# Kernel tuning notes

Hardware: AMD Instinct MI355X
Metric: run time of the kernel (lower is better)

## Reference

```python
import jax, jax.numpy as jnp
import numpy as np

N = 20000        # number of protein atoms
C_IN = 32        # input atom features
C = 128          # hidden_channels
E_BOND = 80000   # directed bond edges (~2 bonds/atom, both directions)
R = 4.0          # radius_graph radius (Angstrom)
BOX = 55.0       # box side -> ~32 neighbors within r=4


def _radius_graph_np(pos, r):
    # symmetric radius graph, no self loops (PyG radius_graph, neighbor cap omitted)
    r2 = r * r
    rows, cols = [], []
    for i0 in range(0, pos.shape[0], 500):
        chunk = pos[i0:i0 + 500]
        d2 = ((chunk[:, None, :] - pos[None, :, :]) ** 2).sum(-1)
        m = d2 < r2
        m[np.arange(chunk.shape[0]), i0 + np.arange(chunk.shape[0])] = False
        ii, jj = np.nonzero(m)
        rows.append(jj)            # source j
        cols.append(ii + i0)       # target i
    return np.stack([np.concatenate(rows), np.concatenate(cols)]).astype(np.int32)


def setup_inputs() -> dict:
    key = jax.random.key(0)
    ks = jax.random.split(key, 12)
    rng = np.random.default_rng(0)

    pos = rng.uniform(0.0, BOX, (N, 3)).astype(np.float32)
    r_edge_index = jnp.asarray(_radius_graph_np(pos, R))

    half = E_BOND // 2
    s = rng.integers(0, N, half); d = rng.integers(0, N, half)
    edge_index = jnp.asarray(np.stack([np.concatenate([s, d]), np.concatenate([d, s])]).astype(np.int32))

    def lin(k, fin, fout):
        lim = 1.0 / np.sqrt(fin)
        kw, kb = jax.random.split(k)
        W = jax.random.uniform(kw, (fin, fout), jnp.float32, -lim, lim)
        b = jax.random.uniform(kb, (fout,), jnp.float32, -lim, lim)
        return W, b

    We1, be1 = lin(ks[0], C_IN, C)
    We2, be2 = lin(ks[1], C, C)
    Wf1, bf1 = lin(ks[2], 2 * C, C); Ws1, bs1 = lin(ks[3], 2 * C, C)
    Wf2, bf2 = lin(ks[4], 2 * C, C); Ws2, bs2 = lin(ks[5], 2 * C, C)
    Wf3, bf3 = lin(ks[6], 2 * C, C); Ws3, bs3 = lin(ks[7], 2 * C, C)
    Wf4, bf4 = lin(ks[8], 2 * C, C); Ws4, bs4 = lin(ks[9], 2 * C, C)

    x_prot = jax.random.normal(ks[10], (N, C_IN), jnp.float32)
    v_prot = jnp.asarray(pos)

    return dict(x_prot=x_prot, v_prot=v_prot, edge_index=edge_index, r_edge_index=r_edge_index,
                We1=We1, be1=be1, We2=We2, be2=be2,
                Wf1=Wf1, bf1=bf1, Ws1=Ws1, bs1=bs1,
                Wf2=Wf2, bf2=bf2, Ws2=Ws2, bs2=bs2,
                Wf3=Wf3, bf3=bf3, Ws3=Ws3, bs3=bs3,
                Wf4=Wf4, bf4=bf4, Ws4=Ws4, bs4=bs4)


def _cgconv(x, ei, Wf, bf, Ws, bs):
    # PyG CGConv: z = [x_i, x_j]; out = x + mean_j sigmoid(lin_f(z)) * softplus(lin_s(z))
    src, dst = ei[0], ei[1]              # source j -> target i
    z = jnp.concatenate([x[dst], x[src]], axis=1)          # [E, 2C]
    msg = jax.nn.sigmoid(z @ Wf + bf) * jax.nn.softplus(z @ Ws + bs)  # [E, C]
    agg = jax.ops.segment_sum(msg, dst, num_segments=x.shape[0])
    cnt = jax.ops.segment_sum(jnp.ones((ei.shape[1],), x.dtype), dst, num_segments=x.shape[0])
    return x + agg / jnp.maximum(cnt, 1.0)[:, None]


def reference(x_prot, v_prot, edge_index, r_edge_index,
              We1, be1, We2, be2,
              Wf1, bf1, Ws1, bs1, Wf2, bf2, Ws2, bs2,
              Wf3, bf3, Ws3, bs3, Wf4, bf4, Ws4, bs4):
    # embed MLP (PyG MLP with batch-norm at init == identity): Linear->ReLU->Linear
    x = jax.nn.relu(x_prot @ We1 + be1) @ We2 + be2
    # bond convs
    x = jax.nn.relu(_cgconv(x, edge_index, Wf1, bf1, Ws1, bs1))
    x = jax.nn.relu(_cgconv(x, edge_index, Wf2, bf2, Ws2, bs2))
    # radius convs (r_edge_index = radius_graph(v_prot, r=4), precomputed in setup)
    x = jax.nn.relu(_cgconv(x, r_edge_index, Wf3, bf3, Ws3, bs3))
    x = jax.nn.relu(_cgconv(x, r_edge_index, Wf4, bf4, Ws4, bs4))
    return jax.nn.relu(x)  # final self.act (idempotent on ReLU output)
```

## Files before the change

kernel.cpp:

```cpp
#include <hip/hip_runtime.h>
#include <hip/hip_bf16.h>

#define NN 20000
#define CC 128

typedef __attribute__((ext_vector_type(8))) _Float16 half8;
typedef __attribute__((ext_vector_type(2))) _Float16 half2v;
typedef __attribute__((ext_vector_type(4))) float f32x4;

typedef const __attribute__((address_space(1))) void gv_t;
typedef __attribute__((address_space(3))) void sv_t;

__global__ __launch_bounds__(256) void conv_all_kernel(
    const float* __restrict__ Wf0, const float* __restrict__ Ws0,
    const float* __restrict__ Wf1, const float* __restrict__ Ws1,
    const float* __restrict__ Wf2, const float* __restrict__ Ws2,
    const float* __restrict__ Wf3, const float* __restrict__ Ws3,
    const float* __restrict__ We2, const float* __restrict__ We1,
    const float* __restrict__ xprot,
    _Float16* __restrict__ WctAll, _Float16* __restrict__ Wcte,
    _Float16* __restrict__ Wt1, _Float16* __restrict__ xp16) {
    int id = blockIdx.x * 256 + threadIdx.x;
    if (id < 262144) {
        int Lw = id >> 16;
        int i = id & 65535;
        int c = i & 511;
        int k = i >> 9;
        const float* Wfp = (Lw == 0) ? Wf0 : (Lw == 1) ? Wf1 : (Lw == 2) ? Wf2 : Wf3;
        const float* Wsp = (Lw == 0) ? Ws0 : (Lw == 1) ? Ws1 : (Lw == 2) ? Ws2 : Ws3;
        float v;
        if (c < 128) v = Wfp[k * 128 + c];
        else if (c < 256) v = Wfp[(128 + k) * 128 + (c - 128)];
        else if (c < 384) v = Wsp[k * 128 + (c - 256)];
        else v = Wsp[(128 + k) * 128 + (c - 384)];
        WctAll[Lw * 65536 + c * 128 + k] = (_Float16)v;
    } else if (id < 278528) {
        int i = id - 262144;
        int c = i & 127;
        int k = i >> 7;
        Wcte[c * 128 + k] = (_Float16)We2[k * 128 + c];
    } else if (id < 282624) {
        int i = id - 278528;
        int c = i & 127;
        int k = i >> 7;
        Wt1[c * 32 + k] = (_Float16)We1[k * 128 + c];
    } else {
        int i = id - 282624;
        xp16[i] = (_Float16)xprot[i];
    }
}

__global__ __launch_bounds__(256) void enc1_mfma_kernel(
    const _Float16* __restrict__ A, const _Float16* __restrict__ Wt1,
    const float* __restrict__ b, _Float16* __restrict__ Y) {
    int t = threadIdx.x;
    int wid = t >> 6, l = t & 63;
    int lr = l & 15, hi = l >> 4;
    int m0 = blockIdx.x * 128 + wid * 32;
    half8 af[2];
#pragma unroll
    for (int m = 0; m < 2; ++m) {
        int row = m0 + m * 16 + lr;
        half8 v = {0, 0, 0, 0, 0, 0, 0, 0};
        if (row < NN) v = *(const half8*)(A + (long)row * 32 + hi * 8);
        af[m] = v;
    }
    f32x4 acc[2][8] = {};
#pragma unroll
    for (int n = 0; n < 8; ++n) {
        int col = n * 16 + lr;
        half8 bg = *(const half8*)(Wt1 + (long)col * 32 + hi * 8);
#pragma unroll
        for (int m = 0; m < 2; ++m)
            acc[m][n] = __builtin_amdgcn_mfma_f32_16x16x32_f16(af[m], bg, acc[m][n], 0, 0, 0);
    }
#pragma unroll
    for (int n = 0; n < 8; ++n) {
        int col = n * 16 + lr;
        float bb = b[col];
#pragma unroll
        for (int m = 0; m < 2; ++m) {
#pragma unroll
            for (int q = 0; q < 4; ++q) {
                int row = m0 + m * 16 + hi * 4 + q;
                if (row < NN)
                    Y[(long)row * 128 + col] = (_Float16)fmaxf(acc[m][n][q] + bb, 0.0f);
            }
        }
    }
}

__global__ __launch_bounds__(256) void gemm_mfma_kernel(
    const _Float16* __restrict__ A, const _Float16* __restrict__ Wt,
    const float* __restrict__ bias0, const float* __restrict__ bias1,
    _Float16* __restrict__ outH, float* __restrict__ outF,
    _Float16* __restrict__ outF16, int M, int mode) {
    __shared__ _Float16 lds[32768];
    int t = threadIdx.x;
    int w = t >> 6, l = t & 63;
    int m0 = blockIdx.x * 128;
    int n0 = blockIdx.y * 128;
    {
        int rin = l >> 4;
        int cs = l & 15;
#pragma unroll
        for (int j = 0; j < 8; ++j) {
            int r = w * 32 + j * 4 + rin;
            int g = cs ^ (r & 7);
            int grow = m0 + r;
            if (grow > M - 1) grow = M - 1;
            const _Float16* srcA = A + (long)grow * 128 + g * 8;
            __builtin_amdgcn_global_load_lds((gv_t*)srcA,
                (sv_t*)&lds[(w * 32 + j * 4) * 128], 16, 0, 0);
            const _Float16* srcB = Wt + (long)(n0 + r) * 128 + g * 8;
            __builtin_amdgcn_global_load_lds((gv_t*)srcB,
                (sv_t*)&lds[16384 + (w * 32 + j * 4) * 128], 16, 0, 0);
        }
    }
    __syncthreads();
    int wm = w >> 1, wn = w & 1;
    int lr = l & 15, hi = l >> 4;
    f32x4 acc[4][4] = {};
#pragma unroll
    for (int ks = 0; ks < 4; ++ks) {
        int cidx = 4 * ks + hi;
        half8 af[4], bg[4];
#pragma unroll
        for (int m = 0; m < 4; ++m) {
            int row = wm * 64 + m * 16 + lr;
            af[m] = *(const half8*)(&lds[row * 128 + (cidx ^ (row & 7)) * 8]);
        }
#pragma unroll
        for (int n = 0; n < 4; ++n) {
            int row = wn * 64 + n * 16 + lr;
            bg[n] = *(const half8*)(&lds[16384 + row * 128 + (cidx ^ (row & 7)) * 8]);
        }
#pragma unroll
        for (int m = 0; m < 4; ++m)
#pragma unroll
            for (int n = 0; n < 4; ++n)
                acc[m][n] = __builtin_amdgcn_mfma_f32_16x16x32_f16(
                    af[m], bg[n], acc[m][n], 0, 0, 0);
    }
    if (mode == 0) {
        __syncthreads();
        const float S = 1.44269504f;
#pragma unroll
        for (int n = 0; n < 4; ++n) {
            int cl = wn * 64 + n * 16 + lr;
            int gcol = n0 + cl;
            float badd = (gcol < 128) ? bias0[gcol]
                       : ((gcol >= 256 && gcol < 384) ? bias1[gcol - 256] : 0.0f);
#pragma unroll
            for (int m = 0; m < 4; ++m)
#pragma unroll
                for (int q = 0; q < 4; ++q) {
                    int rl = wm * 64 + m * 16 + hi * 4 + q;
                    lds[rl * 144 + cl] = (_Float16)((acc[m][n][q] + badd) * S);
                }
        }
        __syncthreads();
#pragma unroll
        for (int i = 0; i < 8; ++i) {
            int id = t + 256 * i;
            int row = id >> 4, ch = id & 15;
            int grow = m0 + row;
            if (grow < M) {
                half8 v = *(const half8*)(&lds[row * 144 + ch * 8]);
                *(half8*)(&outH[(long)grow * 512 + n0 + ch * 8]) = v;
            }
        }
    } else {
#pragma unroll
        for (int n = 0; n < 4; ++n) {
            int gcol = n0 + wn * 64 + n * 16 + lr;
            float badd = bias0[gcol];
#pragma unroll
            for (int m = 0; m < 4; ++m)
#pragma unroll
                for (int q = 0; q < 4; ++q) {
                    int grow = m0 + wm * 64 + m * 16 + hi * 4 + q;
                    if (grow < M) {
                        float v = acc[m][n][q] + badd;
                        outF[(long)grow * 128 + gcol] = v;
                        outF16[(long)grow * 128 + gcol] = (_Float16)v;
                    }
                }
        }
    }
}

__global__ __launch_bounds__(256) void count_int_kernel(
    const int* __restrict__ dst, int E, int* __restrict__ cnt) {
    int e = blockIdx.x * 256 + threadIdx.x;
    if (e < E) atomicAdd(&cnt[dst[e]], 1);
}

__global__ __launch_bounds__(1024) void scan_kernel(
    const int* __restrict__ cnt, int* __restrict__ off) {
    __shared__ int part[1024];
    int t = threadIdx.x;
    int base = t * 20;
    int loc[20];
    int s = 0;
#pragma unroll
    for (int i = 0; i < 20; ++i) {
        int idx = base + i;
        int v = (idx < NN) ? cnt[idx] : 0;
        loc[i] = s;
        s += v;
    }
    part[t] = s;
    __syncthreads();
    for (int d = 1; d < 1024; d <<= 1) {
        int v = (t >= d) ? part[t - d] : 0;
        __syncthreads();
        part[t] += v;
        __syncthreads();
    }
    int pre = (t > 0) ? part[t - 1] : 0;
#pragma unroll
    for (int i = 0; i < 20; ++i) {
        int idx = base + i;
        if (idx < NN) off[idx] = pre + loc[i];
    }
    if (t == 1023) off[NN] = part[1023];
}

__global__ __launch_bounds__(256) void scatter_kernel(
    const int* __restrict__ src, const int* __restrict__ dst, int E,
    const int* __restrict__ off, int* __restrict__ cur, int* __restrict__ eid) {
    int e = blockIdx.x * 256 + threadIdx.x;
    if (e < E) {
        int d = dst[e];
        int p = off[d] + atomicAdd(&cur[d], 1);
        eid[p] = src[e];
    }
}

__global__ __launch_bounds__(256) void csr_off_kernel(
    const int* __restrict__ dst, int E, int N1, int* __restrict__ off) {
    int n = blockIdx.x * 256 + threadIdx.x;
    if (n >= N1) return;
    int lo = 0, hi = E;
    while (lo < hi) {
        int mid = (lo + hi) >> 1;
        if (dst[mid] < n) lo = mid + 1;
        else hi = mid;
    }
    off[n] = lo;
}

__global__ __launch_bounds__(256) void node_agg_kernel(
    const _Float16* __restrict__ H, const int* __restrict__ srcArr,
    const int* __restrict__ off, const float* __restrict__ xin,
    float* __restrict__ xout, _Float16* __restrict__ xh, int write_h) {
    int n = blockIdx.x * 4 + (threadIdx.x >> 6);
    int nu = __builtin_amdgcn_readfirstlane(n);
    int l = threadIdx.x & 63;
    const half2v* H2 = (const half2v*)H;
    const half2v* hrow = H2 + (long)nu * 256;
    half2v fdh = hrow[l];
    half2v sdh = hrow[128 + l];
    int e0 = __builtin_amdgcn_readfirstlane(off[nu]);
    int e1 = __builtin_amdgcn_readfirstlane(off[nu + 1]);
    float ax = 0.0f, ay = 0.0f;
#define EDGEC(fv, sv)                                                         \
    {                                                                         \
        half2v fsum = fdh + (fv);                                             \
        half2v ssum = sdh + (sv);                                             \
        float fx = (float)fsum.x, fy = (float)fsum.y;                         \
        float sx = (float)ssum.x, sy = (float)ssum.y;                         \
        float rx = __builtin_amdgcn_rcpf(1.0f + __builtin_amdgcn_exp2f(-fx)); \
        float ry = __builtin_amdgcn_rcpf(1.0f + __builtin_amdgcn_exp2f(-fy)); \
        float spx = __builtin_amdgcn_logf(1.0f + __builtin_amdgcn_exp2f(sx)); \
        float spy = __builtin_amdgcn_logf(1.0f + __builtin_amdgcn_exp2f(sy)); \
        ax += rx * spx;                                                       \
        ay += ry * spy;                                                       \
    }
    int e = e0;
    for (; e + 7 < e1; e += 8) {
        half2v f[8], g[8];
#pragma unroll
        for (int j = 0; j < 8; ++j) {
            int s = srcArr[e + j];
            const half2v* h = H2 + (long)s * 256;
            f[j] = h[64 + l];
            g[j] = h[192 + l];
        }
#pragma unroll
        for (int j = 0; j < 8; ++j) EDGEC(f[j], g[j])
    }
    for (; e + 1 < e1; e += 2) {
        int s0 = srcArr[e], s1 = srcArr[e + 1];
        const half2v* h0 = H2 + (long)s0 * 256;
        const half2v* h1 = H2 + (long)s1 * 256;
        half2v f0 = h0[64 + l], g0 = h0[192 + l];
        half2v f1 = h1[64 + l], g1 = h1[192 + l];
        EDGEC(f0, g0) EDGEC(f1, g1)
    }
    if (e < e1) {
        int s0 = srcArr[e];
        const half2v* h0 = H2 + (long)s0 * 256;
        half2v f0 = h0[64 + l], g0 = h0[192 + l];
        EDGEC(f0, g0)
    }
#undef EDGEC
    float inv = 0.6931471805599453f *
                __builtin_amdgcn_rcpf(fmaxf((float)(e1 - e0), 1.0f));
    float2 xv = ((const float2*)xin)[(long)nu * 64 + l];
    float ox = fmaxf(xv.x + ax * inv, 0.0f);
    float oy = fmaxf(xv.y + ay * inv, 0.0f);
    ((float2*)xout)[(long)nu * 64 + l] = make_float2(ox, oy);
    if (write_h) {
        half2v oh;
        oh.x = (_Float16)ox;
        oh.y = (_Float16)oy;
        ((half2v*)xh)[(long)nu * 64 + l] = oh;
    }
}

extern "C" void kernel_launch(void* const* d_in, const int* in_sizes, int n_in,
                              void* d_out, int out_size, void* d_ws, size_t ws_size,
                              hipStream_t stream) {
    const float* x_prot = (const float*)d_in[0];
    const int* eb = (const int*)d_in[2];
    const int* er = (const int*)d_in[3];
    int Eb = in_sizes[2] / 2;
    int Er = in_sizes[3] / 2;
    const float* We1 = (const float*)d_in[4];
    const float* be1 = (const float*)d_in[5];
    const float* We2 = (const float*)d_in[6];
    const float* be2 = (const float*)d_in[7];
    const float* Wf[4]  = {(const float*)d_in[8],  (const float*)d_in[12],
                           (const float*)d_in[16], (const float*)d_in[20]};
    const float* bf[4]  = {(const float*)d_in[9],  (const float*)d_in[13],
                           (const float*)d_in[17], (const float*)d_in[21]};
    const float* Wsp[4] = {(const float*)d_in[10], (const float*)d_in[14],
                           (const float*)d_in[18], (const float*)d_in[22]};
    const float* bsp[4] = {(const float*)d_in[11], (const float*)d_in[15],
                           (const float*)d_in[19], (const float*)d_in[23]};

    char* ws = (char*)d_ws;
    float*     xbuf  = (float*)ws;
    _Float16*  xhf   = (_Float16*)(ws + 10240000);
    _Float16*  H     = (_Float16*)(ws + 15360000);
    _Float16*  xp16  = (_Float16*)(ws + 35840000);
    int*       cntI  = (int*)(ws + 37120000);
    int*       curB  = (int*)(ws + 37200000);
    int*       offB  = (int*)(ws + 37280000);
    int*       offR  = (int*)(ws + 37360016);
    int*       eidB  = (int*)(ws + 37440032);
    _Float16*  WctAll= (_Float16*)(ws + 37760032);
    _Float16*  Wcte  = (_Float16*)(ws + 38284320);
    _Float16*  Wt1   = (_Float16*)(ws + 38317088);

    const int* srcB = eb;
    const int* dstB = eb + Eb;
    const int* srcR = er;

    conv_all_kernel<<<3604, 256, 0, stream>>>(
        Wf[0], Wsp[0], Wf[1], Wsp[1], Wf[2], Wsp[2], Wf[3], Wsp[3],
        We2, We1, x_prot, WctAll, Wcte, Wt1, xp16);

    hipMemsetAsync(cntI, 0, 160000, stream);
    count_int_kernel<<<(Eb + 255) / 256, 256, 0, stream>>>(dstB, Eb, cntI);
    scan_kernel<<<1, 1024, 0, stream>>>(cntI, offB);
    scatter_kernel<<<(Eb + 255) / 256, 256, 0, stream>>>(srcB, dstB, Eb, offB, curB, eidB);
    csr_off_kernel<<<(NN + 256) / 256, 256, 0, stream>>>(er + Er, Er, NN + 1, offR);

    enc1_mfma_kernel<<<157, 256, 0, stream>>>(xp16, Wt1, be1, H);
    {
        dim3 g(157, 1);
        gemm_mfma_kernel<<<g, 256, 0, stream>>>(H, Wcte, be2, be2, nullptr,
                                                xbuf, xhf, NN, 1);
    }

    for (int L = 0; L < 4; ++L) {
        dim3 g(157, 4);
        gemm_mfma_kernel<<<g, 256, 0, stream>>>(xhf, WctAll + L * 65536, bf[L],
                                                bsp[L], H, nullptr, nullptr, NN, 0);
        const int* sArr = (L < 2) ? eidB : srcR;
        const int* oArr = (L < 2) ? offB : offR;
        float* xout = (L == 3) ? (float*)d_out : xbuf;
        node_agg_kernel<<<NN / 4, 256, 0, stream>>>(H, sArr, oArr, xbuf, xout,
                                                    xhf, (L == 3) ? 0 : 1);
    }
    (void)n_in; (void)out_size; (void)ws_size;
}
```

Measured before the change: 224.2 us.

## Precompute per-source exp factors in bf16 and factor gate math per edge

The GEMM epilogue now writes the source-side halves of the gate and filter pre-activations as exp2 values rounded to bf16, in a reordered 1024-byte row layout. The node aggregation then computes sigmoid and softplus as rcp(1+ed*es) and log(1+ud*us), with the destination exp computed once per node. This removes two exp2 calls per edge element and reads the B operand directly from global memory into registers with prefetch instead of staging it in LDS, which shrinks the LDS allocation. The risks are bf16 precision on the source factors and possible overflow of the exp values for large pre-activations.

Result: slower. 255.3 us (+13.9%).

```diff
diff --git a/kernel.cpp b/kernel.cpp
--- a/kernel.cpp
+++ b/kernel.cpp
@@ -93,13 +93,22 @@
 __global__ __launch_bounds__(256) void gemm_mfma_kernel(
     const _Float16* __restrict__ A, const _Float16* __restrict__ Wt,
     const float* __restrict__ bias0, const float* __restrict__ bias1,
-    _Float16* __restrict__ outH, float* __restrict__ outF,
+    char* __restrict__ outH, float* __restrict__ outF,
     _Float16* __restrict__ outF16, int M, int mode) {
-    __shared__ _Float16 lds[32768];
+    __shared__ _Float16 lds[18432];
     int t = threadIdx.x;
     int w = t >> 6, l = t & 63;
     int m0 = blockIdx.x * 128;
     int n0 = blockIdx.y * 128;
+    int wm = w >> 1, wn = w & 1;
+    int lr = l & 15, hi = l >> 4;
+    const _Float16* Br[4];
+#pragma unroll
+    for (int n = 0; n < 4; ++n)
+        Br[n] = Wt + (long)(n0 + wn * 64 + n * 16 + lr) * 128 + hi * 8;
+    half8 bcur[4];
+#pragma unroll
+    for (int n = 0; n < 4; ++n) bcur[n] = *(const half8*)(Br[n]);
     {
         int rin = l >> 4;
         int cs = l & 15;
@@ -109,42 +118,43 @@
             int g = cs ^ (r & 7);
             int grow = m0 + r;
             if (grow > M - 1) grow = M - 1;
-            const _Float16* srcA = A + (long)grow * 128 + g * 8;
-            __builtin_amdgcn_global_load_lds((gv_t*)srcA,
+            __builtin_amdgcn_global_load_lds((gv_t*)(A + (long)grow * 128 + g * 8),
                 (sv_t*)&lds[(w * 32 + j * 4) * 128], 16, 0, 0);
-            const _Float16* srcB = Wt + (long)(n0 + r) * 128 + g * 8;
-            __builtin_amdgcn_global_load_lds((gv_t*)srcB,
-                (sv_t*)&lds[16384 + (w * 32 + j * 4) * 128], 16, 0, 0);
         }
     }
     __syncthreads();
-    int wm = w >> 1, wn = w & 1;
-    int lr = l & 15, hi = l >> 4;
     f32x4 acc[4][4] = {};
 #pragma unroll
     for (int ks = 0; ks < 4; ++ks) {
+        half8 bnxt[4];
+        if (ks < 3) {
+#pragma unroll
+            for (int n = 0; n < 4; ++n)
+                bnxt[n] = *(const half8*)(Br[n] + (ks + 1) * 32);
+        }
         int cidx = 4 * ks + hi;
-        half8 af[4], bg[4];
+        half8 af[4];
 #pragma unroll
         for (int m = 0; m < 4; ++m) {
             int row = wm * 64 + m * 16 + lr;
             af[m] = *(const half8*)(&lds[row * 128 + (cidx ^ (row & 7)) * 8]);
         }
 #pragma unroll
-        for (int n = 0; n < 4; ++n) {
-            int row = wn * 64 + n * 16 + lr;
-            bg[n] = *(const half8*)(&lds[16384 + row * 128 + (cidx ^ (row & 7)) * 8]);
-        }
-#pragma unroll
         for (int m = 0; m < 4; ++m)
 #pragma unroll
             for (int n = 0; n < 4; ++n)
                 acc[m][n] = __builtin_amdgcn_mfma_f32_16x16x32_f16(
-                    af[m], bg[n], acc[m][n], 0, 0, 0);
+                    af[m], bcur[n], acc[m][n], 0, 0, 0);
+        if (ks < 3) {
+#pragma unroll
+            for (int n = 0; n < 4; ++n) bcur[n] = bnxt[n];
+        }
     }
     if (mode == 0) {
         __syncthreads();
         const float S = 1.44269504f;
+        bool isSrc = (n0 == 128) || (n0 == 384);
+        float sgn = (n0 == 128) ? -S : S;
 #pragma unroll
         for (int n = 0; n < 4; ++n) {
             int cl = wn * 64 + n * 16 + lr;
@@ -156,10 +166,19 @@
 #pragma unroll
                 for (int q = 0; q < 4; ++q) {
                     int rl = wm * 64 + m * 16 + hi * 4 + q;
-                    lds[rl * 144 + cl] = (_Float16)((acc[m][n][q] + badd) * S);
+                    float v = acc[m][n][q] + badd;
+                    if (!isSrc) {
+                        lds[rl * 144 + cl] = (_Float16)(v * S);
+                    } else {
+                        float p = __builtin_amdgcn_exp2f(v * sgn);
+                        uint b = __float_as_uint(p);
+                        b = (b + 0x7FFFu + ((b >> 16) & 1u)) >> 16;
+                        ((ushort*)lds)[rl * 144 + cl] = (ushort)b;
+                    }
                 }
         }
         __syncthreads();
+        int base = (n0 == 0) ? 0 : (n0 == 128) ? 512 : (n0 == 256) ? 256 : 768;
 #pragma unroll
         for (int i = 0; i < 8; ++i) {
             int id = t + 256 * i;
@@ -167,7 +186,7 @@
             int grow = m0 + row;
             if (grow < M) {
                 half8 v = *(const half8*)(&lds[row * 144 + ch * 8]);
-                *(half8*)(&outH[(long)grow * 512 + n0 + ch * 8]) = v;
+                *(half8*)(outH + (long)grow * 1024 + base + ch * 16) = v;
             }
         }
     } else {
@@ -252,58 +271,54 @@
 }
 
 __global__ __launch_bounds__(256) void node_agg_kernel(
-    const _Float16* __restrict__ H, const int* __restrict__ srcArr,
+    const char* __restrict__ H, const int* __restrict__ srcArr,
     const int* __restrict__ off, const float* __restrict__ xin,
     float* __restrict__ xout, _Float16* __restrict__ xh, int write_h) {
     int n = blockIdx.x * 4 + (threadIdx.x >> 6);
     int nu = __builtin_amdgcn_readfirstlane(n);
     int l = threadIdx.x & 63;
-    const half2v* H2 = (const half2v*)H;
-    const half2v* hrow = H2 + (long)nu * 256;
-    half2v fdh = hrow[l];
-    half2v sdh = hrow[128 + l];
+    const char* hb = H + (long)nu * 1024;
+    half2v fdh = *(const half2v*)(hb + l * 4);
+    half2v sdh = *(const half2v*)(hb + 256 + l * 4);
+    float vd0 = __builtin_amdgcn_exp2f(-(float)fdh.x);
+    float vd1 = __builtin_amdgcn_exp2f(-(float)fdh.y);
+    float ud0 = __builtin_amdgcn_exp2f((float)sdh.x);
+    float ud1 = __builtin_amdgcn_exp2f((float)sdh.y);
     int e0 = __builtin_amdgcn_readfirstlane(off[nu]);
     int e1 = __builtin_amdgcn_readfirstlane(off[nu + 1]);
     float ax = 0.0f, ay = 0.0f;
-#define EDGEC(fv, sv)                                                         \
-    {                                                                         \
-        half2v fsum = fdh + (fv);                                             \
-        half2v ssum = sdh + (sv);                                             \
-        float fx = (float)fsum.x, fy = (float)fsum.y;                         \
-        float sx = (float)ssum.x, sy = (float)ssum.y;                         \
-        float rx = __builtin_amdgcn_rcpf(1.0f + __builtin_amdgcn_exp2f(-fx)); \
-        float ry = __builtin_amdgcn_rcpf(1.0f + __builtin_amdgcn_exp2f(-fy)); \
-        float spx = __builtin_amdgcn_logf(1.0f + __builtin_amdgcn_exp2f(sx)); \
-        float spy = __builtin_amdgcn_logf(1.0f + __builtin_amdgcn_exp2f(sy)); \
-        ax += rx * spx;                                                       \
-        ay += ry * spy;                                                       \
+#define EDGEC(w0, w1)                                                        \
+    {                                                                        \
+        float vs0 = __uint_as_float((w0) << 16);                             \
+        float vs1 = __uint_as_float((w0) & 0xFFFF0000u);                     \
+        float us0 = __uint_as_float((w1) << 16);                             \
+        float us1 = __uint_as_float((w1) & 0xFFFF0000u);                     \
+        float rx = __builtin_amdgcn_rcpf(__builtin_fmaf(vd0, vs0, 1.0f));    \
+        float ry = __builtin_amdgcn_rcpf(__builtin_fmaf(vd1, vs1, 1.0f));    \
+        float px = __builtin_amdgcn_logf(__builtin_fmaf(ud0, us0, 1.0f));    \
+        float py = __builtin_amdgcn_logf(__builtin_fmaf(ud1, us1, 1.0f));    \
+        ax = __builtin_fmaf(rx, px, ax);                                     \
+        ay = __builtin_fmaf(ry, py, ay);                                     \
     }
     int e = e0;
     for (; e + 7 < e1; e += 8) {
-        half2v f[8], g[8];
+        uint wv[8], wu[8];
 #pragma unroll
         for (int j = 0; j < 8; ++j) {
             int s = srcArr[e + j];
-            const half2v* h = H2 + (long)s * 256;
-            f[j] = h[64 + l];
-            g[j] = h[192 + l];
-        }
-#pragma unroll
-        for (int j = 0; j < 8; ++j) EDGEC(f[j], g[j])
-    }
-    for (; e + 1 < e1; e += 2) {
-        int s0 = srcArr[e], s1 = srcArr[e + 1];
-        const half2v* h0 = H2 + (long)s0 * 256;
-        const half2v* h1 = H2 + (long)s1 * 256;
-        half2v f0 = h0[64 + l], g0 = h0[192 + l];
-        half2v f1 = h1[64 + l], g1 = h1[192 + l];
-        EDGEC(f0, g0) EDGEC(f1, g1)
-    }
-    if (e < e1) {
-        int s0 = srcArr[e];
-        const half2v* h0 = H2 + (long)s0 * 256;
-        half2v f0 = h0[64 + l], g0 = h0[192 + l];
-        EDGEC(f0, g0)
+            const char* hs = H + (long)s * 1024 + (long)l * 4;
+            wv[j] = *(const uint*)(hs + 512);
+            wu[j] = *(const uint*)(hs + 768);
+        }
+#pragma unroll
+        for (int j = 0; j < 8; ++j) EDGEC(wv[j], wu[j])
+    }
+    for (; e < e1; ++e) {
+        int s = srcArr[e];
+        const char* hs = H + (long)s * 1024 + (long)l * 4;
+        uint w0 = *(const uint*)(hs + 512);
+        uint w1 = *(const uint*)(hs + 768);
+        EDGEC(w0, w1)
     }
 #undef EDGEC
     float inv = 0.6931471805599453f *
@@ -344,7 +359,7 @@
     char* ws = (char*)d_ws;
     float*     xbuf  = (float*)ws;
     _Float16*  xhf   = (_Float16*)(ws + 10240000);
-    _Float16*  H     = (_Float16*)(ws + 15360000);
+    char*      H     = (char*)(ws + 15360000);
     _Float16*  xp16  = (_Float16*)(ws + 35840000);
     int*       cntI  = (int*)(ws + 37120000);
     int*       curB  = (int*)(ws + 37200000);
@@ -369,11 +384,11 @@
     scatter_kernel<<<(Eb + 255) / 256, 256, 0, stream>>>(srcB, dstB, Eb, offB, curB, eidB);
     csr_off_kernel<<<(NN + 256) / 256, 256, 0, stream>>>(er + Er, Er, NN + 1, offR);
 
-    enc1_mfma_kernel<<<157, 256, 0, stream>>>(xp16, Wt1, be1, H);
+    enc1_mfma_kernel<<<157, 256, 0, stream>>>(xp16, Wt1, be1, (_Float16*)H);
     {
         dim3 g(157, 1);
-        gemm_mfma_kernel<<<g, 256, 0, stream>>>(H, Wcte, be2, be2, nullptr,
-                                                xbuf, xhf, NN, 1);
+        gemm_mfma_kernel<<<g, 256, 0, stream>>>((_Float16*)H, Wcte, be2, be2,
+                                                nullptr, xbuf, xhf, NN, 1);
     }
 
     for (int L = 0; L < 4; ++L) {
```
